# Optimization experiments

Hardware: AMD Instinct MI355X
Metric: run time of the kernel (lower is better)

## Reference

```python
import jax, jax.numpy as jnp
import numpy as np

N_HEADS = 16
D_HEAD = 64
QUERY_DIM = 1024
CONTEXT_DIM = 1024
INNER = N_HEADS * D_HEAD


def setup_inputs() -> dict:
    key = jax.random.key(0)
    ks = jax.random.split(key, 7)
    B, Nq, Nk = 4, 1024, 1024
    x = jax.random.normal(ks[0], (B, Nq, QUERY_DIM), dtype=jnp.float32)
    context = jax.random.normal(ks[1], (B, Nk, CONTEXT_DIM), dtype=jnp.float32)
    s_q = 1.0 / np.sqrt(QUERY_DIM)
    s_c = 1.0 / np.sqrt(CONTEXT_DIM)
    s_i = 1.0 / np.sqrt(INNER)
    Wq = jax.random.uniform(ks[2], (QUERY_DIM, INNER), jnp.float32, -s_q, s_q)
    Wk = jax.random.uniform(ks[3], (CONTEXT_DIM, INNER), jnp.float32, -s_c, s_c)
    Wv = jax.random.uniform(ks[4], (CONTEXT_DIM, INNER), jnp.float32, -s_c, s_c)
    Wo = jax.random.uniform(ks[5], (INNER, QUERY_DIM), jnp.float32, -s_i, s_i)
    bo = jax.random.uniform(ks[6], (QUERY_DIM,), jnp.float32, -s_i, s_i)
    return {"x": x, "context": context, "Wq": Wq, "Wk": Wk, "Wv": Wv, "Wo": Wo, "bo": bo}


def reference(x, context, Wq, Wk, Wv, Wo, bo):
    B, Nq, _ = x.shape
    Nk = context.shape[1]
    scale = D_HEAD ** -0.5
    # project and split heads: [B, H, N, d]
    q = (x @ Wq).reshape(B, Nq, N_HEADS, D_HEAD).transpose(0, 2, 1, 3)
    k = (context @ Wk).reshape(B, Nk, N_HEADS, D_HEAD).transpose(0, 2, 1, 3)
    v = (context @ Wv).reshape(B, Nk, N_HEADS, D_HEAD).transpose(0, 2, 1, 3)
    scores = jnp.einsum("bhqd,bhkd->bhqk", q, k) * scale
    attn = jax.nn.softmax(scores, axis=-1)
    out = jnp.einsum("bhqk,bhkd->bhqd", attn, v)
    out = out.transpose(0, 2, 1, 3).reshape(B, Nq, INNER)
    return out @ Wo + bo
```

## Files before the change

kernel.cpp:

```cpp
#include <hip/hip_runtime.h>
#include <hip/hip_bf16.h>

#define BATCH 4
#define NQ 1024
#define NKK 1024
#define HD 1024
#define NHEADS 16

typedef __bf16 bf16x8 __attribute__((ext_vector_type(8)));
typedef float f32x4 __attribute__((ext_vector_type(4)));
typedef unsigned short u16;
typedef unsigned int u32;

__device__ __forceinline__ u16 f2bf(float f) {
    union { __bf16 h; u16 u; } v;
    v.h = (__bf16)f;
    return v.u;
}

#define GLOAD16(gp, lp) \
    __builtin_amdgcn_global_load_lds((const __attribute__((address_space(1))) void*)(gp), \
                                     (__attribute__((address_space(3))) void*)(lp), 16, 0, 0)

#define MFMA16(a, b, c) __builtin_amdgcn_mfma_f32_16x16x32_bf16(a, b, c, 0, 0, 0)

__global__ __launch_bounds__(256) void cvt2bf_k(const float* __restrict__ a,
                                                u16* __restrict__ o, int n4) {
    int i = blockIdx.x * blockDim.x + threadIdx.x;
    const int stride = gridDim.x * blockDim.x;
    for (; i < n4; i += stride) {
        float4 v = ((const float4*)a)[i];
        ushort4 p;
        p.x = f2bf(v.x); p.y = f2bf(v.y); p.z = f2bf(v.z); p.w = f2bf(v.w);
        ((ushort4*)o)[i] = p;
    }
}

__global__ __launch_bounds__(256) void transpose4_k(const float* __restrict__ w0,
                                                    const float* __restrict__ w1,
                                                    const float* __restrict__ w2,
                                                    const float* __restrict__ w3,
                                                    u16* __restrict__ ws) {
    const float* src = blockIdx.z == 0 ? w0 : blockIdx.z == 1 ? w1 : blockIdx.z == 2 ? w2 : w3;
    const float scl = (blockIdx.z == 0) ? 0.18033688011112042f : 1.0f;
    u16* dst = ws + (size_t)blockIdx.z * (1024u * 1024u);
    __shared__ u16 t[64][65];
    const int bx = blockIdx.x * 64;
    const int by = blockIdx.y * 64;
    const int tid = threadIdx.x;
#pragma unroll
    for (int p = 0; p < 16; ++p) {
        int idx = p * 256 + tid;
        int r = idx >> 6, c = idx & 63;
        t[c][r] = f2bf(scl * src[(size_t)(by + r) * 1024 + bx + c]);
    }
    __syncthreads();
#pragma unroll
    for (int p = 0; p < 16; ++p) {
        int idx = p * 256 + tid;
        int r = idx >> 6, c = idx & 63;
        dst[(size_t)(bx + r) * 1024 + by + c] = t[r][c];
    }
}

__global__ __launch_bounds__(256) void gemm_qkv(const u16* __restrict__ Xb,
                                                const u16* __restrict__ Cb,
                                                const u16* __restrict__ WqT,
                                                const u16* __restrict__ WkT,
                                                const u16* __restrict__ WvT,
                                                u16* __restrict__ Qb,
                                                u16* __restrict__ Kb,
                                                u16* __restrict__ VTb) {
    const int bid = blockIdx.x;
    const int swz = (bid & 7) * 192 + (bid >> 3);
    const int z = swz / 512;
    const int rem = swz - z * 512;
    const int m0 = (rem >> 3) * 64;
    const int n0 = (rem & 7) * 128;

    const u16* __restrict__ A  = (z == 0) ? Xb : Cb;
    const u16* __restrict__ BT = (z == 0) ? WqT : (z == 1) ? WkT : WvT;

    __shared__ __align__(16) u16 Asm[64 * 64];
    __shared__ __align__(16) u16 Bsm[128 * 64];

    const int tid = threadIdx.x, lane = tid & 63, wv = tid >> 6;
    const int wm = wv >> 1, wn = wv & 1;
    const int lr = lane & 15, lg = lane >> 4;
    const int lx = lr & 7;
    const int M = BATCH * NQ, N = HD, K = HD;

    f32x4 acc[2][4];
#pragma unroll
    for (int i = 0; i < 2; ++i)
#pragma unroll
        for (int j = 0; j < 4; ++j) acc[i][j] = (f32x4)(0.0f);

    for (int kt = 0; kt < K; kt += 64) {
        __syncthreads();
#pragma unroll
        for (int i = 0; i < 2; ++i) {
            const int cb = (wv * 2 + i) * 64;
            const int s = cb + lane;
            const int row = s >> 3, cg = (s & 7) ^ (row & 7);
            GLOAD16(A + (size_t)(m0 + row) * K + kt + cg * 8, &Asm[cb * 8]);
        }
#pragma unroll
        for (int i = 0; i < 4; ++i) {
            const int cb = (wv * 4 + i) * 64;
            const int s = cb + lane;
            const int row = s >> 3, cg = (s & 7) ^ (row & 7);
            GLOAD16(BT + (size_t)(n0 + row) * K + kt + cg * 8, &Bsm[cb * 8]);
        }
        __syncthreads();
        bf16x8 af[2][2], bfr[4][2];
#pragma unroll
        for (int m = 0; m < 2; ++m)
#pragma unroll
            for (int kk = 0; kk < 2; ++kk)
                af[m][kk] = *(const bf16x8*)&Asm[((wm * 32 + m * 16 + lr) * 8 +
                                                 ((kk * 4 + lg) ^ lx)) * 8];
#pragma unroll
        for (int n = 0; n < 4; ++n)
#pragma unroll
            for (int kk = 0; kk < 2; ++kk)
                bfr[n][kk] = *(const bf16x8*)&Bsm[((wn * 64 + n * 16 + lr) * 8 +
                                                  ((kk * 4 + lg) ^ lx)) * 8];
#pragma unroll
        for (int kk = 0; kk < 2; ++kk)
#pragma unroll
            for (int m = 0; m < 2; ++m)
#pragma unroll
                for (int n = 0; n < 4; ++n)
                    acc[m][n] = MFMA16(af[m][kk], bfr[n][kk], acc[m][n]);
    }

    if (z < 2) {
        u16* __restrict__ C = (z == 0) ? Qb : Kb;
#pragma unroll
        for (int m = 0; m < 2; ++m)
#pragma unroll
            for (int n = 0; n < 4; ++n) {
                const int col = n0 + wn * 64 + n * 16 + lr;
                const int rb = m0 + wm * 32 + m * 16 + lg * 4;
#pragma unroll
                for (int r = 0; r < 4; ++r)
                    C[(size_t)(rb + r) * N + col] = f2bf(acc[m][n][r]);
            }
    } else {
#pragma unroll
        for (int m = 0; m < 2; ++m)
#pragma unroll
            for (int n = 0; n < 4; ++n) {
                const int col = n0 + wn * 64 + n * 16 + lr;
                const int rb = m0 + wm * 32 + m * 16 + lg * 4;
                ushort4 pk;
                pk.x = f2bf(acc[m][n][0]);
                pk.y = f2bf(acc[m][n][1]);
                pk.z = f2bf(acc[m][n][2]);
                pk.w = f2bf(acc[m][n][3]);
                *(ushort4*)&VTb[(size_t)col * M + rb] = pk;
            }
    }
}

__global__ __launch_bounds__(256) void gemm_out(const u16* __restrict__ A,
                                                const u16* __restrict__ BT,
                                                const float* __restrict__ bias,
                                                float* __restrict__ C) {
    const int bid = blockIdx.x;
    const int swz = (bid & 7) * 64 + (bid >> 3);
    const int m0 = (swz >> 3) * 64;
    const int n0 = (swz & 7) * 128;

    __shared__ __align__(16) u16 Asm[64 * 64];
    __shared__ __align__(16) u16 Bsm[128 * 64];

    const int tid = threadIdx.x, lane = tid & 63, wv = tid >> 6;
    const int wm = wv >> 1, wn = wv & 1;
    const int lr = lane & 15, lg = lane >> 4;
    const int lx = lr & 7;
    const int N = HD, K = HD;

    f32x4 acc[2][4];
#pragma unroll
    for (int i = 0; i < 2; ++i)
#pragma unroll
        for (int j = 0; j < 4; ++j) acc[i][j] = (f32x4)(0.0f);

    for (int kt = 0; kt < K; kt += 64) {
        __syncthreads();
#pragma unroll
        for (int i = 0; i < 2; ++i) {
            const int cb = (wv * 2 + i) * 64;
            const int s = cb + lane;
            const int row = s >> 3, cg = (s & 7) ^ (row & 7);
            GLOAD16(A + (size_t)(m0 + row) * K + kt + cg * 8, &Asm[cb * 8]);
        }
#pragma unroll
        for (int i = 0; i < 4; ++i) {
            const int cb = (wv * 4 + i) * 64;
            const int s = cb + lane;
            const int row = s >> 3, cg = (s & 7) ^ (row & 7);
            GLOAD16(BT + (size_t)(n0 + row) * K + kt + cg * 8, &Bsm[cb * 8]);
        }
        __syncthreads();
        bf16x8 af[2][2], bfr[4][2];
#pragma unroll
        for (int m = 0; m < 2; ++m)
#pragma unroll
            for (int kk = 0; kk < 2; ++kk)
                af[m][kk] = *(const bf16x8*)&Asm[((wm * 32 + m * 16 + lr) * 8 +
                                                 ((kk * 4 + lg) ^ lx)) * 8];
#pragma unroll
        for (int n = 0; n < 4; ++n)
#pragma unroll
            for (int kk = 0; kk < 2; ++kk)
                bfr[n][kk] = *(const bf16x8*)&Bsm[((wn * 64 + n * 16 + lr) * 8 +
                                                  ((kk * 4 + lg) ^ lx)) * 8];
#pragma unroll
        for (int kk = 0; kk < 2; ++kk)
#pragma unroll
            for (int m = 0; m < 2; ++m)
#pragma unroll
                for (int n = 0; n < 4; ++n)
                    acc[m][n] = MFMA16(af[m][kk], bfr[n][kk], acc[m][n]);
    }

#pragma unroll
    for (int m = 0; m < 2; ++m)
#pragma unroll
        for (int n = 0; n < 4; ++n) {
            const int col = n0 + wn * 64 + n * 16 + lr;
            const int rb = m0 + wm * 32 + m * 16 + lg * 4;
            const float bv = bias[col];
#pragma unroll
            for (int r = 0; r < 4; ++r)
                C[(size_t)(rb + r) * N + col] = acc[m][n][r] + bv;
        }
}

__global__ __launch_bounds__(256) void attn_k(const u16* __restrict__ Q,
                                              const u16* __restrict__ Kp,
                                              const u16* __restrict__ VT,
                                              u16* __restrict__ AO) {
    __shared__ __align__(16) u16 Ksm[2][64 * 64];
    __shared__ __align__(16) u16 Vsm[2][64 * 64];
    __shared__ __align__(16) u16 Psm[4][16 * 64];

    const int tid = threadIdx.x, lane = tid & 63, wv = tid >> 6;
    const int lr = lane & 15, lg = lane >> 4;

    const int swz = (blockIdx.x & 7) * 128 + (blockIdx.x >> 3);
    const int bh = swz >> 4;
    const int b = bh >> 4, h = bh & 15;
    const int q0 = (swz & 15) * 64 + wv * 16;
    const int lx = lr & 7;

    bf16x8 qf[2];
#pragma unroll
    for (int ks = 0; ks < 2; ++ks)
        qf[ks] = *(const bf16x8*)&Q[(size_t)(b * NQ + q0 + lr) * HD +
                                    h * 64 + ks * 32 + lg * 8];

    const int kbase = b * NKK, vrow0 = h * 64;
    auto stageKV = [&](int kt, int bufsel) {
#pragma unroll
        for (int i = 0; i < 2; ++i) {
            const int cb = (wv * 2 + i) * 64;
            const int s = cb + lane;
            const int row = s >> 3;
            const int cg = (s & 7) ^ (row & 7);
            GLOAD16(Kp + (size_t)(kbase + kt + row) * HD + h * 64 + cg * 8,
                    &Ksm[bufsel][cb * 8]);
            GLOAD16(VT + (size_t)(vrow0 + row) * (BATCH * NKK) + kbase + kt + cg * 8,
                    &Vsm[bufsel][cb * 8]);
        }
    };

    float sum[4] = {0.0f, 0.0f, 0.0f, 0.0f};
    f32x4 o[4];
#pragma unroll
    for (int n = 0; n < 4; ++n) o[n] = (f32x4)(0.0f);

    stageKV(0, 0);
    __syncthreads();
    int cur = 0;

    for (int t = 0; t < NKK / 64; ++t) {
        if (t + 1 < NKK / 64) stageKV((t + 1) * 64, cur ^ 1);
        const u16* Ks = &Ksm[cur][0];
        const u16* Vs = &Vsm[cur][0];

        f32x4 s[4];
#pragma unroll
        for (int n = 0; n < 4; ++n) s[n] = (f32x4)(0.0f);
#pragma unroll
        for (int n = 0; n < 4; ++n) {
            bf16x8 kf0 = *(const bf16x8*)&Ks[(n * 16 + lr) * 64 + (lg ^ lx) * 8];
            bf16x8 kf1 = *(const bf16x8*)&Ks[(n * 16 + lr) * 64 + ((lg | 4) ^ lx) * 8];
            s[n] = MFMA16(qf[0], kf0, s[n]);
            s[n] = MFMA16(qf[1], kf1, s[n]);
        }

        u16* P = &Psm[wv][0];
#pragma unroll
        for (int n = 0; n < 4; ++n)
#pragma unroll
            for (int r = 0; r < 4; ++r) {
                const float p = exp2f(s[n][r]);
                sum[r] += p;
                const int row = lg * 4 + r;
                const int c = n * 2 + (lr >> 3);
                P[row * 64 + ((c ^ (row & 7)) * 8) + (lr & 7)] = f2bf(p);
            }

#pragma unroll
        for (int ks = 0; ks < 2; ++ks) {
            bf16x8 pa = *(const bf16x8*)&P[lr * 64 + (((ks * 4 + lg) ^ lx)) * 8];
#pragma unroll
            for (int n = 0; n < 4; ++n) {
                bf16x8 vf = *(const bf16x8*)&Vs[(n * 16 + lr) * 64 + (((ks * 4 + lg) ^ lx)) * 8];
                o[n] = MFMA16(pa, vf, o[n]);
            }
        }
        __syncthreads();
        cur ^= 1;
    }

    float rs[4];
#pragma unroll
    for (int r = 0; r < 4; ++r) {
        float v = sum[r];
#pragma unroll
        for (int d = 1; d < 16; d <<= 1) v += __shfl_xor(v, d);
        rs[r] = 1.0f / v;
    }

#pragma unroll
    for (int n = 0; n < 4; ++n)
#pragma unroll
        for (int r = 0; r < 4; ++r) {
            const float v = o[n][r] * rs[r];
            AO[(size_t)(b * NQ + q0 + lg * 4 + r) * HD +
               h * 64 + n * 16 + lr] = f2bf(v);
        }
}

extern "C" void kernel_launch(void* const* d_in, const int* in_sizes, int n_in,
                              void* d_out, int out_size, void* d_ws, size_t ws_size,
                              hipStream_t stream) {
    const float* x   = (const float*)d_in[0];
    const float* ctx = (const float*)d_in[1];
    const float* Wq  = (const float*)d_in[2];
    const float* Wk  = (const float*)d_in[3];
    const float* Wv  = (const float*)d_in[4];
    const float* Wo  = (const float*)d_in[5];
    const float* bo  = (const float*)d_in[6];

    u16* ws = (u16*)d_ws;
    const size_t MEG = 1024u * 1024u;
    u16* WqT = ws + 0 * MEG;
    u16* WkT = ws + 1 * MEG;
    u16* WvT = ws + 2 * MEG;
    u16* WoT = ws + 3 * MEG;
    u16* Xb  = ws + 4 * MEG;
    u16* Cb  = ws + 8 * MEG;
    u16* Qb  = ws + 12 * MEG;
    u16* Kb  = ws + 16 * MEG;
    u16* VTb = ws + 20 * MEG;
    u16* AOb = Xb;

    transpose4_k<<<dim3(16, 16, 4), 256, 0, stream>>>(Wq, Wk, Wv, Wo, ws);
    cvt2bf_k<<<4096, 256, 0, stream>>>(x,   Xb, 1024 * 1024);
    cvt2bf_k<<<4096, 256, 0, stream>>>(ctx, Cb, 1024 * 1024);
    gemm_qkv<<<1536, 256, 0, stream>>>(Xb, Cb, WqT, WkT, WvT, Qb, Kb, VTb);
    attn_k<<<1024, 256, 0, stream>>>(Qb, Kb, VTb, AOb);
    gemm_out<<<512, 256, 0, stream>>>(AOb, WoT, bo, (float*)d_out);
}
```

Baseline: 107.5 us.

## Enlarge QKV GEMM and attention tiles to 128 rows per block

The QKV projection GEMM moves from 64x128 to 128x128 tiles, halving the grid and doubling MFMA work per staged LDS tile. The attention kernel gives each wave 32 query rows instead of 16, so each K/V tile loaded into LDS is reused across twice as many queries. It also computes S transposed, which lets P be written with packed ushort4 stores and changes how the row-sum reduction is done. s_setprio is placed around the MFMA blocks; in exchange, higher register pressure and fewer blocks may lower occupancy.

```diff
diff --git a/kernel.cpp b/kernel.cpp
--- a/kernel.cpp
+++ b/kernel.cpp
@@ -72,16 +72,16 @@
                                                 u16* __restrict__ Kb,
                                                 u16* __restrict__ VTb) {
     const int bid = blockIdx.x;
-    const int swz = (bid & 7) * 192 + (bid >> 3);
-    const int z = swz / 512;
-    const int rem = swz - z * 512;
-    const int m0 = (rem >> 3) * 64;
+    const int swz = (bid & 7) * 96 + (bid >> 3);
+    const int z = swz >> 8;
+    const int rem = swz & 255;
+    const int m0 = (rem >> 3) * 128;
     const int n0 = (rem & 7) * 128;
 
     const u16* __restrict__ A  = (z == 0) ? Xb : Cb;
     const u16* __restrict__ BT = (z == 0) ? WqT : (z == 1) ? WkT : WvT;
 
-    __shared__ __align__(16) u16 Asm[64 * 64];
+    __shared__ __align__(16) u16 Asm[128 * 64];
     __shared__ __align__(16) u16 Bsm[128 * 64];
 
     const int tid = threadIdx.x, lane = tid & 63, wv = tid >> 6;
@@ -90,70 +90,61 @@
     const int lx = lr & 7;
     const int M = BATCH * NQ, N = HD, K = HD;
 
-    f32x4 acc[2][4];
-#pragma unroll
-    for (int i = 0; i < 2; ++i)
+    f32x4 acc[4][4];
+#pragma unroll
+    for (int i = 0; i < 4; ++i)
 #pragma unroll
         for (int j = 0; j < 4; ++j) acc[i][j] = (f32x4)(0.0f);
 
     for (int kt = 0; kt < K; kt += 64) {
         __syncthreads();
-#pragma unroll
-        for (int i = 0; i < 2; ++i) {
-            const int cb = (wv * 2 + i) * 64;
-            const int s = cb + lane;
-            const int row = s >> 3, cg = (s & 7) ^ (row & 7);
-            GLOAD16(A + (size_t)(m0 + row) * K + kt + cg * 8, &Asm[cb * 8]);
-        }
 #pragma unroll
         for (int i = 0; i < 4; ++i) {
             const int cb = (wv * 4 + i) * 64;
             const int s = cb + lane;
             const int row = s >> 3, cg = (s & 7) ^ (row & 7);
+            GLOAD16(A + (size_t)(m0 + row) * K + kt + cg * 8, &Asm[cb * 8]);
             GLOAD16(BT + (size_t)(n0 + row) * K + kt + cg * 8, &Bsm[cb * 8]);
         }
         __syncthreads();
-        bf16x8 af[2][2], bfr[4][2];
-#pragma unroll
-        for (int m = 0; m < 2; ++m)
-#pragma unroll
-            for (int kk = 0; kk < 2; ++kk)
-                af[m][kk] = *(const bf16x8*)&Asm[((wm * 32 + m * 16 + lr) * 8 +
-                                                 ((kk * 4 + lg) ^ lx)) * 8];
-#pragma unroll
-        for (int n = 0; n < 4; ++n)
-#pragma unroll
-            for (int kk = 0; kk < 2; ++kk)
-                bfr[n][kk] = *(const bf16x8*)&Bsm[((wn * 64 + n * 16 + lr) * 8 +
-                                                  ((kk * 4 + lg) ^ lx)) * 8];
-#pragma unroll
-        for (int kk = 0; kk < 2; ++kk)
-#pragma unroll
-            for (int m = 0; m < 2; ++m)
+#pragma unroll
+        for (int kk = 0; kk < 2; ++kk) {
+            bf16x8 af[4], bfr[4];
+#pragma unroll
+            for (int m = 0; m < 4; ++m)
+                af[m] = *(const bf16x8*)&Asm[((wm * 64 + m * 16 + lr) * 8 +
+                                             ((kk * 4 + lg) ^ lx)) * 8];
+#pragma unroll
+            for (int n = 0; n < 4; ++n)
+                bfr[n] = *(const bf16x8*)&Bsm[((wn * 64 + n * 16 + lr) * 8 +
+                                              ((kk * 4 + lg) ^ lx)) * 8];
+#pragma unroll
+            for (int m = 0; m < 4; ++m)
 #pragma unroll
                 for (int n = 0; n < 4; ++n)
-                    acc[m][n] = MFMA16(af[m][kk], bfr[n][kk], acc[m][n]);
+                    acc[m][n] = MFMA16(af[m], bfr[n], acc[m][n]);
+        }
     }
 
     if (z < 2) {
         u16* __restrict__ C = (z == 0) ? Qb : Kb;
 #pragma unroll
-        for (int m = 0; m < 2; ++m)
+        for (int m = 0; m < 4; ++m)
 #pragma unroll
             for (int n = 0; n < 4; ++n) {
                 const int col = n0 + wn * 64 + n * 16 + lr;
-                const int rb = m0 + wm * 32 + m * 16 + lg * 4;
+                const int rb = m0 + wm * 64 + m * 16 + lg * 4;
 #pragma unroll
                 for (int r = 0; r < 4; ++r)
                     C[(size_t)(rb + r) * N + col] = f2bf(acc[m][n][r]);
             }
     } else {
 #pragma unroll
-        for (int m = 0; m < 2; ++m)
+        for (int m = 0; m < 4; ++m)
 #pragma unroll
             for (int n = 0; n < 4; ++n) {
                 const int col = n0 + wn * 64 + n * 16 + lr;
-                const int rb = m0 + wm * 32 + m * 16 + lg * 4;
+                const int rb = m0 + wm * 64 + m * 16 + lg * 4;
                 ushort4 pk;
                 pk.x = f2bf(acc[m][n][0]);
                 pk.y = f2bf(acc[m][n][1]);
@@ -246,22 +237,24 @@
                                               u16* __restrict__ AO) {
     __shared__ __align__(16) u16 Ksm[2][64 * 64];
     __shared__ __align__(16) u16 Vsm[2][64 * 64];
-    __shared__ __align__(16) u16 Psm[4][16 * 64];
+    __shared__ __align__(16) u16 Psm[4][32 * 64];
 
     const int tid = threadIdx.x, lane = tid & 63, wv = tid >> 6;
     const int lr = lane & 15, lg = lane >> 4;
 
-    const int swz = (blockIdx.x & 7) * 128 + (blockIdx.x >> 3);
-    const int bh = swz >> 4;
+    const int swz = (blockIdx.x & 7) * 64 + (blockIdx.x >> 3);
+    const int bh = swz >> 3;
     const int b = bh >> 4, h = bh & 15;
-    const int q0 = (swz & 15) * 64 + wv * 16;
+    const int q0 = (swz & 7) * 128 + wv * 32;
     const int lx = lr & 7;
 
-    bf16x8 qf[2];
-#pragma unroll
-    for (int ks = 0; ks < 2; ++ks)
-        qf[ks] = *(const bf16x8*)&Q[(size_t)(b * NQ + q0 + lr) * HD +
-                                    h * 64 + ks * 32 + lg * 8];
+    bf16x8 qf[2][2];
+#pragma unroll
+    for (int mq = 0; mq < 2; ++mq)
+#pragma unroll
+        for (int ks = 0; ks < 2; ++ks)
+            qf[mq][ks] = *(const bf16x8*)&Q[(size_t)(b * NQ + q0 + mq * 16 + lr) * HD +
+                                            h * 64 + ks * 32 + lg * 8];
 
     const int kbase = b * NKK, vrow0 = h * 64;
     auto stageKV = [&](int kt, int bufsel) {
@@ -278,10 +271,12 @@
         }
     };
 
-    float sum[4] = {0.0f, 0.0f, 0.0f, 0.0f};
-    f32x4 o[4];
-#pragma unroll
-    for (int n = 0; n < 4; ++n) o[n] = (f32x4)(0.0f);
+    float sum[2] = {0.0f, 0.0f};
+    f32x4 o[2][4];
+#pragma unroll
+    for (int mq = 0; mq < 2; ++mq)
+#pragma unroll
+        for (int n = 0; n < 4; ++n) o[mq][n] = (f32x4)(0.0f);
 
     stageKV(0, 0);
     __syncthreads();
@@ -291,60 +286,82 @@
         if (t + 1 < NKK / 64) stageKV((t + 1) * 64, cur ^ 1);
         const u16* Ks = &Ksm[cur][0];
         const u16* Vs = &Vsm[cur][0];
-
-        f32x4 s[4];
-#pragma unroll
-        for (int n = 0; n < 4; ++n) s[n] = (f32x4)(0.0f);
-#pragma unroll
-        for (int n = 0; n < 4; ++n) {
-            bf16x8 kf0 = *(const bf16x8*)&Ks[(n * 16 + lr) * 64 + (lg ^ lx) * 8];
-            bf16x8 kf1 = *(const bf16x8*)&Ks[(n * 16 + lr) * 64 + ((lg | 4) ^ lx) * 8];
-            s[n] = MFMA16(qf[0], kf0, s[n]);
-            s[n] = MFMA16(qf[1], kf1, s[n]);
-        }
-
         u16* P = &Psm[wv][0];
+
+        f32x4 s[4][2];
+#pragma unroll
+        for (int kn = 0; kn < 4; ++kn)
+#pragma unroll
+            for (int mq = 0; mq < 2; ++mq) s[kn][mq] = (f32x4)(0.0f);
+        __builtin_amdgcn_s_setprio(1);
+#pragma unroll
+        for (int kn = 0; kn < 4; ++kn) {
+            bf16x8 kf0 = *(const bf16x8*)&Ks[(kn * 16 + lr) * 64 + (lg ^ lx) * 8];
+            bf16x8 kf1 = *(const bf16x8*)&Ks[(kn * 16 + lr) * 64 + ((lg | 4) ^ lx) * 8];
+#pragma unroll
+            for (int mq = 0; mq < 2; ++mq) {
+                s[kn][mq] = MFMA16(kf0, qf[mq][0], s[kn][mq]);
+                s[kn][mq] = MFMA16(kf1, qf[mq][1], s[kn][mq]);
+            }
+        }
+        __builtin_amdgcn_s_setprio(0);
+
+#pragma unroll
+        for (int mq = 0; mq < 2; ++mq)
+#pragma unroll
+            for (int kn = 0; kn < 4; ++kn) {
+                const float p0 = exp2f(s[kn][mq][0]);
+                const float p1 = exp2f(s[kn][mq][1]);
+                const float p2 = exp2f(s[kn][mq][2]);
+                const float p3 = exp2f(s[kn][mq][3]);
+                sum[mq] += (p0 + p1) + (p2 + p3);
+                ushort4 pk;
+                pk.x = f2bf(p0); pk.y = f2bf(p1); pk.z = f2bf(p2); pk.w = f2bf(p3);
+                const int ch = (2 * kn + (lg >> 1)) ^ lx;
+                *(ushort4*)&P[(mq * 16 + lr) * 64 + ch * 8 + (lg & 1) * 4] = pk;
+            }
+
+#pragma unroll
+        for (int ks = 0; ks < 2; ++ks) {
+            bf16x8 pa[2], vf[4];
+#pragma unroll
+            for (int mq = 0; mq < 2; ++mq)
+                pa[mq] = *(const bf16x8*)&P[(mq * 16 + lr) * 64 + (((ks * 4 + lg) ^ lx)) * 8];
+#pragma unroll
+            for (int n = 0; n < 4; ++n)
+                vf[n] = *(const bf16x8*)&Vs[(n * 16 + lr) * 64 + (((ks * 4 + lg) ^ lx)) * 8];
+            __builtin_amdgcn_s_setprio(1);
+#pragma unroll
+            for (int mq = 0; mq < 2; ++mq)
+#pragma unroll
+                for (int n = 0; n < 4; ++n)
+                    o[mq][n] = MFMA16(pa[mq], vf[n], o[mq][n]);
+            __builtin_amdgcn_s_setprio(0);
+        }
+        __syncthreads();
+        cur ^= 1;
+    }
+
+    float v0 = sum[0], v1 = sum[1];
+    v0 += __shfl_xor(v0, 16); v0 += __shfl_xor(v0, 32);
+    v1 += __shfl_xor(v1, 16); v1 += __shfl_xor(v1, 32);
+    float rs[2][4];
+#pragma unroll
+    for (int r = 0; r < 4; ++r) {
+        rs[0][r] = 1.0f / __shfl(v0, lg * 4 + r);
+        rs[1][r] = 1.0f / __shfl(v1, lg * 4 + r);
+    }
+
+#pragma unroll
+    for (int mq = 0; mq < 2; ++mq)
 #pragma unroll
         for (int n = 0; n < 4; ++n)
 #pragma unroll
             for (int r = 0; r < 4; ++r) {
-                const float p = exp2f(s[n][r]);
-                sum[r] += p;
-                const int row = lg * 4 + r;
-                const int c = n * 2 + (lr >> 3);
-                P[row * 64 + ((c ^ (row & 7)) * 8) + (lr & 7)] = f2bf(p);
-            }
-
-#pragma unroll
-        for (int ks = 0; ks < 2; ++ks) {
-            bf16x8 pa = *(const bf16x8*)&P[lr * 64 + (((ks * 4 + lg) ^ lx)) * 8];
-#pragma unroll
-            for (int n = 0; n < 4; ++n) {
-                bf16x8 vf = *(const bf16x8*)&Vs[(n * 16 + lr) * 64 + (((ks * 4 + lg) ^ lx)) * 8];
-                o[n] = MFMA16(pa, vf, o[n]);
-            }
-        }
-        __syncthreads();
-        cur ^= 1;
-    }
-
-    float rs[4];
-#pragma unroll
-    for (int r = 0; r < 4; ++r) {
-        float v = sum[r];
-#pragma unroll
-        for (int d = 1; d < 16; d <<= 1) v += __shfl_xor(v, d);
-        rs[r] = 1.0f / v;
-    }
-
-#pragma unroll
-    for (int n = 0; n < 4; ++n)
-#pragma unroll
-        for (int r = 0; r < 4; ++r) {
-            const float v = o[n][r] * rs[r];
-            AO[(size_t)(b * NQ + q0 + lg * 4 + r) * HD +
-               h * 64 + n * 16 + lr] = f2bf(v);
-        }
+                const float val = o[mq][n][r] * rs[mq][r];
+                AO[(size_t)(b * NQ + q0 + mq * 16 + lg * 4 + r) * HD +
+                   h * 64 + n * 16 + lr] = f2bf(val);
+            }
 }
 
 extern "C" void kernel_launch(void* const* d_in, const int* in_sizes, int n_in,
@@ -374,7 +391,7 @@
     transpose4_k<<<dim3(16, 16, 4), 256, 0, stream>>>(Wq, Wk, Wv, Wo, ws);
     cvt2bf_k<<<4096, 256, 0, stream>>>(x,   Xb, 1024 * 1024);
     cvt2bf_k<<<4096, 256, 0, stream>>>(ctx, Cb, 1024 * 1024);
-    gemm_qkv<<<1536, 256, 0, stream>>>(Xb, Cb, WqT, WkT, WvT, Qb, Kb, VTb);
-    attn_k<<<1024, 256, 0, stream>>>(Qb, Kb, VTb, AOb);
+    gemm_qkv<<<768, 256, 0, stream>>>(Xb, Cb, WqT, WkT, WvT, Qb, Kb, VTb);
+    attn_k<<<512, 256, 0, stream>>>(Qb, Kb, VTb, AOb);
     gemm_out<<<512, 256, 0, stream>>>(AOb, WoT, bo, (float*)d_out);
 }
```

New measurement: 115.0 us. +7.0%, slower.
